# Kernel tuning notes

Measured on AMD Instinct MI355X. Metric: run time of the kernel, lower is better.

## Reference

```python
import jax, jax.numpy as jnp
import numpy as np

K, D, BETA = 512, 64, 0.25


def conv(x, w, b, s, p):
    # x: NCHW, w: OIHW (torch Conv2d layout)
    y = jax.lax.conv_general_dilated(x, w, (s, s), [(p, p), (p, p)],
                                     dimension_numbers=('NCHW', 'OIHW', 'NCHW'))
    if b is not None:
        y = y + b[None, :, None, None]
    return y


def conv_t(x, w, b, s, p):
    # torch ConvTranspose2d: w is (Cin, Cout, k, k). Equivalent to a dilated conv
    # with flipped, transposed kernel and padding k-1-p.
    k = w.shape[2]
    w2 = jnp.transpose(jnp.flip(w, (2, 3)), (1, 0, 2, 3))  # -> (Cout, Cin, k, k)
    y = jax.lax.conv_general_dilated(x, w2, (1, 1), [(k - 1 - p, k - 1 - p)] * 2,
                                     lhs_dilation=(s, s),
                                     dimension_numbers=('NCHW', 'OIHW', 'NCHW'))
    return y + b[None, :, None, None]


def res_stack(x, w1s, w2s):
    # w1s: (n_blocks, C_mid, C_in, 3, 3); w2s: (n_blocks, C_in, C_mid, 1, 1); no bias
    for i in range(w1s.shape[0]):
        h = conv(jax.nn.relu(x), w1s[i], None, 1, 1)
        h = conv(jax.nn.relu(h), w2s[i], None, 1, 0)
        x = x + h
    return jax.nn.relu(x)


def setup_inputs() -> dict:
    key = jax.random.key(0)
    ks = jax.random.split(key, 24)
    rn = lambda k, shape, s=0.05: (jax.random.normal(k, shape, jnp.float32) * s)
    return {
        'x': jax.random.normal(ks[0], (64, 3, 128, 128), jnp.float32),
        'enc_w1': rn(ks[1], (64, 3, 4, 4)),    'enc_b1': rn(ks[2], (64,)),
        'enc_w2': rn(ks[3], (128, 64, 4, 4)),  'enc_b2': rn(ks[4], (128,)),
        'enc_w3': rn(ks[5], (128, 128, 3, 3)), 'enc_b3': rn(ks[6], (128,)),
        'enc_w4': rn(ks[7], (128, 128, 3, 3)), 'enc_b4': rn(ks[8], (128,)),
        'enc_res_w1': rn(ks[9], (2, 64, 128, 3, 3)),
        'enc_res_w2': rn(ks[10], (2, 128, 64, 1, 1)),
        'enc_adj_w': rn(ks[11], (64, 128, 1, 1)), 'enc_adj_b': rn(ks[12], (64,)),
        'E': jax.random.uniform(ks[13], (K, D), jnp.float32, -1.0 / K, 1.0 / K),
        'dec_adj_w': rn(ks[14], (128, 64, 3, 3)), 'dec_adj_b': rn(ks[15], (128,)),
        'dec_res_w1': rn(ks[16], (2, 64, 128, 3, 3)),
        'dec_res_w2': rn(ks[17], (2, 128, 64, 1, 1)),
        'tc1_w': rn(ks[18], (128, 64, 4, 4)), 'tc1_b': rn(ks[19], (64,)),
        'tc2_w': rn(ks[20], (64, 3, 4, 4)),  'tc2_b': rn(ks[21], (3,)),
    }


def vq_vae_forward(x, enc_w1, enc_b1, enc_w2, enc_b2, enc_w3, enc_b3, enc_w4, enc_b4,
                   enc_res_w1, enc_res_w2, enc_adj_w, enc_adj_b, E,
                   dec_adj_w, dec_adj_b, dec_res_w1, dec_res_w2, tc1_w, tc1_b, tc2_w, tc2_b):
    relu = jax.nn.relu
    # ---- Encoder ----
    h = relu(conv(x, enc_w1, enc_b1, 2, 1))      # (B,64,64,64)
    h = relu(conv(h, enc_w2, enc_b2, 2, 1))      # (B,128,32,32)
    h = relu(conv(h, enc_w3, enc_b3, 1, 1))
    h = conv(h, enc_w4, enc_b4, 1, 1)
    h = res_stack(h, enc_res_w1, enc_res_w2)
    Ze = conv(h, enc_adj_w, enc_adj_b, 1, 0)     # (B,D,32,32)
    # ---- Vector quantizer (eval mode, use_EMA=False) ----
    Zt = jnp.transpose(Ze, (0, 2, 3, 1))          # (B,H,W,D)
    flat = Zt.reshape(-1, D)                      # (N,D), N=65536
    dist = (jnp.sum(flat ** 2, axis=1, keepdims=True)
            + jnp.sum(E ** 2, axis=1)
            - 2.0 * flat @ E.T)                    # (N,K)
    idx = jnp.argmin(dist, axis=1)                # (N,)
    Zq = E[idx].reshape(Zt.shape)
    e_latent_loss = jnp.mean((jax.lax.stop_gradient(Zq) - Zt) ** 2)
    q_latent_loss = jnp.mean((Zq - jax.lax.stop_gradient(Zt)) ** 2)
    e_and_q = q_latent_loss + BETA * e_latent_loss
    Zq_st = Zt + jax.lax.stop_gradient(Zq - Zt)   # straight-through
    Zq_nchw = jnp.transpose(Zq_st, (0, 3, 1, 2))
    counts = jnp.zeros((K,), jnp.float32).at[idx].add(1.0)
    probs = counts / jnp.sum(counts)
    entropy_bits = -jnp.sum(probs * jnp.log2(probs + 1e-10))  # zero-count terms vanish
    est_words = 2.0 ** entropy_bits
    # ---- Decoder ----
    g = conv(Zq_nchw, dec_adj_w, dec_adj_b, 1, 1)  # (B,128,32,32)
    g = res_stack(g, dec_res_w1, dec_res_w2)
    g = relu(conv_t(g, tc1_w, tc1_b, 2, 1))        # (B,64,64,64)
    x_recon = conv_t(g, tc2_w, tc2_b, 2, 1)        # (B,3,128,128)
    return e_and_q, x_recon, e_latent_loss, q_latent_loss, est_words


def reference(x, enc_w1, enc_b1, enc_w2, enc_b2, enc_w3, enc_b3, enc_w4, enc_b4,
              enc_res_w1, enc_res_w2, enc_adj_w, enc_adj_b, E,
              dec_adj_w, dec_adj_b, dec_res_w1, dec_res_w2, tc1_w, tc1_b, tc2_w, tc2_b):
    return vq_vae_forward(x, enc_w1, enc_b1, enc_w2, enc_b2, enc_w3, enc_b3, enc_w4, enc_b4,
                          enc_res_w1, enc_res_w2, enc_adj_w, enc_adj_b, E,
                          dec_adj_w, dec_adj_b, dec_res_w1, dec_res_w2, tc1_w, tc1_b, tc2_w, tc2_b)
```

## Files before the change

### kernel.cpp

```cpp
#include <hip/hip_runtime.h>
#include <math.h>


typedef unsigned short u16;
typedef __attribute__((ext_vector_type(8))) short bf16x8;
typedef __attribute__((ext_vector_type(4))) float f32x4;

__device__ __forceinline__ float bf2f(u16 h) {
    union { unsigned u; float f; } v; v.u = ((unsigned)h) << 16; return v.f;
}
__device__ __forceinline__ u16 f2bf(float f) {
    union { float f; unsigned u; } v; v.f = f;
    unsigned r = v.u + 0x7FFFu + ((v.u >> 16) & 1u);
    return (u16)(r >> 16);
}
__device__ __forceinline__ unsigned relu2(unsigned x) {
    return x & ~(((x & 0x80008000u) >> 15) * 0xFFFFu);
}
__device__ __forceinline__ int swz512(int x) {
    return ((x & 7) << 6) | (x >> 3);
}

template<int CIN, int COUT, int TAPMODE, bool RELU_IN, bool RELU_OUT,
         bool HAS_BIAS, bool RESID>
__global__ __launch_bounds__(256)
void mfma_conv_k(const u16* __restrict__ in, const u16* __restrict__ wT,
                 const float* __restrict__ bias, u16* __restrict__ out,
                 int Hin, int Win, int Hout, int Wout, int OS)
{
    constexpr int TM = 2, TN = 4;
    constexpr int LDA = 40;
    constexpr int NCH = CIN / 32;
    constexpr int NTAPS = (TAPMODE == 0) ? 1 : (TAPMODE == 1) ? 9
                        : (TAPMODE == 2) ? 16 : 4;
    constexpr int S = (TAPMODE == 2) ? 2 : 1;

    __shared__ alignas(16) u16 aT[128 * LDA];
    __shared__ alignas(16) u16 bT[64 * LDA];

    const int tid = threadIdx.x;
    const int m0 = swz512(blockIdx.x) * 128;
    const int colbase = blockIdx.y << 6;
    const int pz = (TAPMODE == 3) ? blockIdx.z : 0;
    const u16* wTb = (TAPMODE == 3) ? wT + (size_t)pz * 4 * COUT * CIN : wT;
    const int oph = (TAPMODE == 3) ? (pz >> 1) : 0;
    const int opw = (TAPMODE == 3) ? (pz & 1) : 0;
    const int n_img = m0 >> 10;
    const int pixbase = m0 & 1023;

    const int r = tid >> 1, half = tid & 1;
    const int pr = pixbase + r;
    const int ohr = pr >> 5, owr = pr & 31;
    const u16* inb = in + (size_t)n_img * Hin * Win * CIN;

    const int wv = tid >> 6, lane = tid & 63;
    const int q = lane >> 4, l16 = lane & 15;
    const int mbase = wv * 32;
    const bool bload = r < 64;

    f32x4 acc[TM][TN] = {};

    const int total_it = NTAPS * NCH;
    uint4 pa0, pa1, pb0 = {0,0,0,0}, pb1 = {0,0,0,0};

#define LOAD_IT(IT) do {                                                        \
        int t_ = (IT) / NCH, cc_ = ((IT) % NCH) * 32;                           \
        int dh_, dw_;                                                           \
        if (TAPMODE == 0)      { dh_ = 0;              dw_ = 0; }               \
        else if (TAPMODE == 1) { dh_ = t_/3 - 1;       dw_ = t_%3 - 1; }        \
        else if (TAPMODE == 2) { dh_ = (t_>>2) - 1;    dw_ = (t_&3) - 1; }      \
        else                   { dh_ = (pz>>1) - (t_>>1); dw_ = (pz&1) - (t_&1); } \
        int ih_ = ohr * S + dh_;                                                \
        int iw_ = owr * S + dw_;                                                \
        bool ok_ = ((unsigned)ih_ < (unsigned)Hin) &&                           \
                   ((unsigned)iw_ < (unsigned)Win);                             \
        pa0 = (uint4){0,0,0,0}; pa1 = (uint4){0,0,0,0};                         \
        if (ok_) {                                                              \
            const u16* as_ = inb + ((size_t)ih_ * Win + iw_) * CIN              \
                             + half * 16 + cc_;                                 \
            pa0 = *(const uint4*)(as_);                                         \
            pa1 = *(const uint4*)(as_ + 8);                                     \
        }                                                                       \
        if (bload) {                                                            \
            const u16* bs_ = wTb + ((size_t)t_ * COUT + colbase + r) * CIN      \
                             + half * 16 + cc_;                                 \
            pb0 = *(const uint4*)(bs_);                                         \
            pb1 = *(const uint4*)(bs_ + 8);                                     \
        }                                                                       \
    } while (0)

    LOAD_IT(0);

    for (int it = 0; it < total_it; ++it) {
        __syncthreads();
        uint4 a0 = pa0, a1 = pa1;
        if (RELU_IN) {
            a0.x = relu2(a0.x); a0.y = relu2(a0.y); a0.z = relu2(a0.z); a0.w = relu2(a0.w);
            a1.x = relu2(a1.x); a1.y = relu2(a1.y); a1.z = relu2(a1.z); a1.w = relu2(a1.w);
        }
        *(uint4*)&aT[r * LDA + half * 16]     = a0;
        *(uint4*)&aT[r * LDA + half * 16 + 8] = a1;
        if (bload) {
            *(uint4*)&bT[r * LDA + half * 16]     = pb0;
            *(uint4*)&bT[r * LDA + half * 16 + 8] = pb1;
        }
        __syncthreads();
        if (it + 1 < total_it) LOAD_IT(it + 1);

        bf16x8 afr[TM], bfr[TN];
        #pragma unroll
        for (int tm = 0; tm < TM; ++tm)
            afr[tm] = *(const bf16x8*)&aT[(mbase + tm*16 + l16) * LDA + q * 8];
        #pragma unroll
        for (int tn = 0; tn < TN; ++tn)
            bfr[tn] = *(const bf16x8*)&bT[(tn*16 + l16) * LDA + q * 8];
        #pragma unroll
        for (int tm = 0; tm < TM; ++tm)
            #pragma unroll
            for (int tn = 0; tn < TN; ++tn)
                acc[tm][tn] = __builtin_amdgcn_mfma_f32_16x16x32_bf16(
                    afr[tm], bfr[tn], acc[tm][tn], 0, 0, 0);
    }
#undef LOAD_IT

    #pragma unroll
    for (int tm = 0; tm < TM; ++tm) {
        #pragma unroll
        for (int tn = 0; tn < TN; ++tn) {
            const int col = colbase + tn*16 + l16;
            const float bv = HAS_BIAS ? bias[col] : 0.0f;
            #pragma unroll
            for (int rg = 0; rg < 4; ++rg) {
                const int m = mbase + tm*16 + q*4 + rg;
                const int pix = pixbase + m;
                const int oh = pix >> 5, ow = pix & 31;
                size_t oidx = (((size_t)n_img * Hout + (oh*OS + oph)) * Wout
                               + (ow*OS + opw)) * COUT + col;
                float v = acc[tm][tn][rg] + bv;
                if (RESID) v += bf2f(out[oidx]);
                if (RELU_OUT) v = fmaxf(v, 0.0f);
                out[oidx] = f2bf(v);
            }
        }
    }
}

template<bool FRELU>
__global__ __launch_bounds__(256)
void res_fused_k(const u16* __restrict__ in, const u16* __restrict__ w1,
                 const u16* __restrict__ w2, u16* __restrict__ out)
{
    constexpr int LDA = 40;
    __shared__ alignas(16) u16 smem[20480];
    u16* aT   = smem;
    u16* bT   = smem + 5120;
    u16* mT0  = smem;
    u16* mT1  = smem + 5120;
    u16* b2T0 = smem + 10240;
    u16* b2T1 = smem + 15360;

    const int tid = threadIdx.x;
    const int m0 = swz512(blockIdx.x) * 128;
    const int n_img = m0 >> 10;
    const int pixbase = m0 & 1023;

    const int r = tid >> 1, half = tid & 1;
    const int pr = pixbase + r;
    const int ohr = pr >> 5, owr = pr & 31;
    const u16* inb = in + (size_t)n_img * 1024 * 128;

    const int wv = tid >> 6, lane = tid & 63;
    const int q = lane >> 4, l16 = lane & 15;
    const int mbase = wv * 32;
    const bool bload = r < 64;

    {
        const u16* s = w2 + r * 64 + half * 32;
        u16* d = (half ? b2T1 : b2T0) + r * LDA;
        *(uint4*)(d)      = *(const uint4*)(s);
        *(uint4*)(d + 8)  = *(const uint4*)(s + 8);
        *(uint4*)(d + 16) = *(const uint4*)(s + 16);
        *(uint4*)(d + 24) = *(const uint4*)(s + 24);
    }

    f32x4 acc[2][4] = {};
    uint4 pa0, pa1, pb0 = {0,0,0,0}, pb1 = {0,0,0,0};

#define RLOAD(IT) do {                                                          \
        int t_ = (IT) >> 2, cc_ = ((IT) & 3) * 32;                              \
        int ih_ = ohr + t_/3 - 1, iw_ = owr + t_%3 - 1;                         \
        bool ok_ = ((unsigned)ih_ < 32u) && ((unsigned)iw_ < 32u);              \
        pa0 = (uint4){0,0,0,0}; pa1 = (uint4){0,0,0,0};                         \
        if (ok_) {                                                              \
            const u16* as_ = inb + ((size_t)ih_ * 32 + iw_) * 128               \
                             + half * 16 + cc_;                                 \
            pa0 = *(const uint4*)(as_);                                         \
            pa1 = *(const uint4*)(as_ + 8);                                     \
        }                                                                       \
        if (bload) {                                                            \
            const u16* bs_ = w1 + ((size_t)t_ * 64 + r) * 128                   \
                             + half * 16 + cc_;                                 \
            pb0 = *(const uint4*)(bs_);                                         \
            pb1 = *(const uint4*)(bs_ + 8);                                     \
        }                                                                       \
    } while (0)

    RLOAD(0);
    for (int it = 0; it < 36; ++it) {
        __syncthreads();
        uint4 a0 = pa0, a1 = pa1;
        a0.x = relu2(a0.x); a0.y = relu2(a0.y); a0.z = relu2(a0.z); a0.w = relu2(a0.w);
        a1.x = relu2(a1.x); a1.y = relu2(a1.y); a1.z = relu2(a1.z); a1.w = relu2(a1.w);
        *(uint4*)&aT[r * LDA + half * 16]     = a0;
        *(uint4*)&aT[r * LDA + half * 16 + 8] = a1;
        if (bload) {
            *(uint4*)&bT[r * LDA + half * 16]     = pb0;
            *(uint4*)&bT[r * LDA + half * 16 + 8] = pb1;
        }
        __syncthreads();
        if (it + 1 < 36) RLOAD(it + 1);

        bf16x8 afr[2], bfr[4];
        #pragma unroll
        for (int tm = 0; tm < 2; ++tm)
            afr[tm] = *(const bf16x8*)&aT[(mbase + tm*16 + l16) * LDA + q * 8];
        #pragma unroll
        for (int tn = 0; tn < 4; ++tn)
            bfr[tn] = *(const bf16x8*)&bT[(tn*16 + l16) * LDA + q * 8];
        #pragma unroll
        for (int tm = 0; tm < 2; ++tm)
            #pragma unroll
            for (int tn = 0; tn < 4; ++tn)
                acc[tm][tn] = __builtin_amdgcn_mfma_f32_16x16x32_bf16(
                    afr[tm], bfr[tn], acc[tm][tn], 0, 0, 0);
    }
#undef RLOAD

    __syncthreads();

    #pragma unroll
    for (int tm = 0; tm < 2; ++tm)
        #pragma unroll
        for (int tn = 0; tn < 4; ++tn) {
            u16* dst = (tn < 2) ? mT0 : mT1;
            const int kc = (tn & 1) * 16 + l16;
            #pragma unroll
            for (int rg = 0; rg < 4; ++rg) {
                int row = mbase + tm*16 + q*4 + rg;
                dst[row * LDA + kc] = f2bf(fmaxf(acc[tm][tn][rg], 0.0f));
            }
        }
    __syncthreads();

    f32x4 acc2[2][8] = {};
    #pragma unroll
    for (int kk = 0; kk < 2; ++kk) {
        const u16* mp = kk ? mT1 : mT0;
        const u16* bp = kk ? b2T1 : b2T0;
        bf16x8 af[2], bf[8];
        #pragma unroll
        for (int tm = 0; tm < 2; ++tm)
            af[tm] = *(const bf16x8*)&mp[(mbase + tm*16 + l16) * LDA + q * 8];
        #pragma unroll
        for (int tn = 0; tn < 8; ++tn)
            bf[tn] = *(const bf16x8*)&bp[(tn*16 + l16) * LDA + q * 8];
        #pragma unroll
        for (int tm = 0; tm < 2; ++tm)
            #pragma unroll
            for (int tn = 0; tn < 8; ++tn)
                acc2[tm][tn] = __builtin_amdgcn_mfma_f32_16x16x32_bf16(
                    af[tm], bf[tn], acc2[tm][tn], 0, 0, 0);
    }

    #pragma unroll
    for (int tm = 0; tm < 2; ++tm)
        #pragma unroll
        for (int tn = 0; tn < 8; ++tn) {
            const int col = tn*16 + l16;
            #pragma unroll
            for (int rg = 0; rg < 4; ++rg) {
                const int m = mbase + tm*16 + q*4 + rg;
                const int pix = pixbase + m;
                size_t off = ((size_t)n_img * 1024 + pix) * 128 + col;
                float v = acc2[tm][tn][rg] + bf2f(in[off]);
                if (FRELU) v = fmaxf(v, 0.0f);
                out[off] = f2bf(v);
            }
        }
}

__global__ __launch_bounds__(256)
void adjvq_k(const u16* __restrict__ TRin, const u16* __restrict__ wadj,
             const float* __restrict__ bias, const u16* __restrict__ Ebf,
             const float* __restrict__ enorm1, u16* __restrict__ Zq,
             u16* __restrict__ idx_out, float* __restrict__ sse)
{
    constexpr int LDA = 40;
    __shared__ alignas(16) u16 smem[18432];
    u16* aT  = smem;
    u16* bT  = smem + 5120;
    u16* mT0 = smem;
    u16* mT1 = smem + 5120;
    u16* eld = smem;
    __shared__ float znorm_s[128];
    __shared__ float bestf_s[128];
    __shared__ float en1s[256];
    __shared__ int   bestk_s[128];
    __shared__ float red[256];

    const int tid = threadIdx.x;
    const int r = tid >> 1, half = tid & 1;
    const int bx = swz512(blockIdx.x);
    const size_t gp = (size_t)bx * 128 + r;
    const u16* arow = TRin + gp * 128 + half * 16;
    const u16* brow = wadj + (size_t)r * 128 + half * 16;

    const int wv = tid >> 6, lane = tid & 63;
    const int q = lane >> 4, l16 = lane & 15;
// ... 213 lines not shown
    #pragma unroll
    for (int tm = 0; tm < 2; ++tm) {
        af0[tm] = *(const bf16x8*)&aT0[(mbase + tm*16 + l16) * 40 + q * 8];
        af1[tm] = *(const bf16x8*)&aT1[(mbase + tm*16 + l16) * 40 + q * 8];
    }
    #pragma unroll
    for (int tn = 0; tn < 4; ++tn) {
        bf0[tn] = *(const bf16x8*)&bT0[(tn*16 + l16) * 40 + q * 8];
        bf1[tn] = *(const bf16x8*)&bT1[(tn*16 + l16) * 40 + q * 8];
    }
    #pragma unroll
    for (int tm = 0; tm < 2; ++tm)
        #pragma unroll
        for (int tn = 0; tn < 4; ++tn) {
            acc[tm][tn] = __builtin_amdgcn_mfma_f32_16x16x32_bf16(
                af0[tm], bf0[tn], acc[tm][tn], 0, 0, 0);
            acc[tm][tn] = __builtin_amdgcn_mfma_f32_16x16x32_bf16(
                af1[tm], bf1[tn], acc[tm][tn], 0, 0, 0);
        }

    float bv[4];
    #pragma unroll
    for (int tn = 0; tn < 4; ++tn) bv[tn] = b[tn*16 + l16];

    __syncthreads();
    u16* cbuf = smem;
    #pragma unroll
    for (int tm = 0; tm < 2; ++tm)
        #pragma unroll
        for (int tn = 0; tn < 4; ++tn)
            #pragma unroll
            for (int rg = 0; rg < 4; ++rg) {
                int row = mbase + tm*16 + q*4 + rg;
                int col = tn*16 + l16;
                cbuf[row*72 + col] = f2bf(fmaxf(acc[tm][tn][rg] + bv[tn], 0.0f));
            }
    __syncthreads();

    u16* ob = out + (size_t)gbase * 64;
    #pragma unroll
    for (int it = 0; it < 4; ++it) {
        int j = it * 256 + tid;
        uint4 v = *(const uint4*)&cbuf[(j >> 3) * 72 + (j & 7) * 8];
        *(uint4*)(ob + j * 8) = v;
    }
}

__global__ __launch_bounds__(256)
void tc2_mfma_k(const u16* __restrict__ in, const u16* __restrict__ wT,
                const float* __restrict__ bias, float* __restrict__ out)
{
    constexpr int LDA = 40;
    __shared__ alignas(16) u16 aT[128 * LDA];
    __shared__ alignas(16) u16 bT[16 * LDA];
    __shared__ float cT[128 * 17];

    const int tid = threadIdx.x;
    const int m0 = blockIdx.x * 128;
    const int n_img = m0 >> 12;
    const int pixbase = m0 & 4095;
    const int y0 = pixbase >> 6;

    const int r = tid >> 1, half = tid & 1;
    const int pr = pixbase + r;
    const int yr = pr >> 6, xr = pr & 63;
    const u16* inb = in + (size_t)n_img * 4096 * 64;

    const int wv = tid >> 6, lane = tid & 63;
    const int q = lane >> 4, l16 = lane & 15;
    const int mbase = wv * 32;

    f32x4 acc[2] = {};

    for (int t = 0; t < 9; ++t) {
        const int ih = yr + t/3 - 1;
        const int iw = xr + t%3 - 1;
        const bool ok = ((unsigned)ih < 64u) && ((unsigned)iw < 64u);
        const u16* asrc = ok ? (inb + ((size_t)ih * 64 + iw) * 64 + half * 16) : inb;
        const u16* bsrc = wT + ((size_t)t * 16 + r) * 64 + half * 16;

        for (int c0 = 0; c0 < 64; c0 += 32) {
            __syncthreads();
            uint4 a0 = {0,0,0,0}, a1 = {0,0,0,0};
            if (ok) {
                a0 = *(const uint4*)(asrc + c0);
                a1 = *(const uint4*)(asrc + c0 + 8);
            }
            *(uint4*)&aT[r * LDA + half * 16]     = a0;
            *(uint4*)&aT[r * LDA + half * 16 + 8] = a1;
            if (r < 16) {
                *(uint4*)&bT[r * LDA + half * 16]     = *(const uint4*)(bsrc + c0);
                *(uint4*)&bT[r * LDA + half * 16 + 8] = *(const uint4*)(bsrc + c0 + 8);
            }
            __syncthreads();

            bf16x8 af0 = *(const bf16x8*)&aT[(mbase + l16) * LDA + q * 8];
            bf16x8 af1 = *(const bf16x8*)&aT[(mbase + 16 + l16) * LDA + q * 8];
            bf16x8 bf  = *(const bf16x8*)&bT[l16 * LDA + q * 8];
            acc[0] = __builtin_amdgcn_mfma_f32_16x16x32_bf16(af0, bf, acc[0], 0, 0, 0);
            acc[1] = __builtin_amdgcn_mfma_f32_16x16x32_bf16(af1, bf, acc[1], 0, 0, 0);
        }
    }

    #pragma unroll
    for (int tm = 0; tm < 2; ++tm)
        #pragma unroll
        for (int rg = 0; rg < 4; ++rg)
            cT[(mbase + tm*16 + q*4 + rg) * 17 + l16] = acc[tm][rg];
    __syncthreads();

    #pragma unroll
    for (int it = 0; it < 6; ++it) {
        int j = it * 256 + tid;
        int co  = j >> 9;
        int rem = j & 511;
        int ohl = rem >> 7;
        int ow  = rem & 127;
        int oh  = 2*y0 + ohl;
        int lp  = (ohl >> 1) * 64 + (ow >> 1);
        int col = ((ohl & 1) * 2 + (ow & 1)) * 4 + co;
        float v = cT[lp * 17 + col] + bias[co];
        out[(((size_t)n_img * 3 + co) * 128 + oh) * 128 + ow] = v;
    }
}

__global__ __launch_bounds__(256)
void hist_k(const u16* __restrict__ idx, float* __restrict__ counts)
{
    __shared__ int red[256];
    const int k = blockIdx.x;
    const int tid = threadIdx.x;
    int c = 0;
    const uint4* p4 = (const uint4*)idx;
    for (int i = tid; i < 8192; i += 256) {
        uint4 v = p4[i];
        unsigned ua[4] = {v.x, v.y, v.z, v.w};
        #pragma unroll
        for (int j = 0; j < 4; ++j) {
            c += ((ua[j] & 0xFFFFu) == (unsigned)k);
            c += ((ua[j] >> 16)     == (unsigned)k);
        }
    }
    red[tid] = c;
    __syncthreads();
    for (int s = 128; s > 0; s >>= 1) {
        if (tid < s) red[tid] += red[tid + s];
        __syncthreads();
    }
    if (tid == 0) counts[k] = (float)red[0];
}

__device__ __forceinline__ void wconv_tf(const float* __restrict__ w,
                                         u16* __restrict__ o,
                                         int COUT, int CIN, int KK, int i)
{
    int ci = i % CIN; int t = i / CIN; int co = t % COUT; t /= COUT;
// ... 122 lines not shown
    const float* enc_b2    = (const float*)d_in[4];
    const float* enc_w3    = (const float*)d_in[5];
    const float* enc_b3    = (const float*)d_in[6];
    const float* enc_w4    = (const float*)d_in[7];
    const float* enc_b4    = (const float*)d_in[8];
    const float* enc_res_w1= (const float*)d_in[9];
    const float* enc_res_w2= (const float*)d_in[10];
    const float* enc_adj_w = (const float*)d_in[11];
    const float* enc_adj_b = (const float*)d_in[12];
    const float* Ecb       = (const float*)d_in[13];
    const float* dec_adj_w = (const float*)d_in[14];
    const float* dec_adj_b = (const float*)d_in[15];
    const float* dec_res_w1= (const float*)d_in[16];
    const float* dec_res_w2= (const float*)d_in[17];
    const float* tc1_w     = (const float*)d_in[18];
    const float* tc1_b     = (const float*)d_in[19];
    const float* tc2_w     = (const float*)d_in[20];
    const float* tc2_b     = (const float*)d_in[21];

    char* wsb = (char*)d_ws;
    u16*   wc2   = (u16*)(wsb + 0);
    u16*   wc3   = (u16*)(wsb + 262144);
    u16*   wc4   = (u16*)(wsb + 557056);
    u16*   wer1  = (u16*)(wsb + 851968);
    u16*   wer2  = (u16*)(wsb + 1146880);
    u16*   weadj = (u16*)(wsb + 1179648);
    u16*   wdadj = (u16*)(wsb + 1196032);
    u16*   wdr1  = (u16*)(wsb + 1343488);
    u16*   wdr2  = (u16*)(wsb + 1638400);
    u16*   wtc1  = (u16*)(wsb + 1671168);
    u16*   wtc2b = (u16*)(wsb + 1933312);
    float* counts= (float*)(wsb + 1951744);
    float* sse   = counts + 512;
    u16*   Ebf   = (u16*)(wsb + 1955840);
    float* enorm1= (float*)(wsb + 2021376);
    u16*   wc1b  = (u16*)(wsb + 2023424);
    u16*   H1    = (u16*)(wsb + 2097152);
    u16*   TR    = (u16*)(wsb + 35651584);
    u16*   H3    = (u16*)(wsb + 52428800);
    u16*   ZQ    = (u16*)(wsb + 85983232);
    u16*   IDX   = (u16*)(wsb + 94371840);
    u16*   TC1O  = H1;

    float* out  = (float*)d_out;
    float* xrec = out + 1;
    float* tail = out + 1 + 3145728;

    prep_k<<<3831, 256, 0, stream>>>(enc_w1, enc_w2, enc_w3, enc_w4,
        enc_res_w1, enc_res_w2, dec_res_w1, dec_res_w2, enc_adj_w, dec_adj_w,
        tc1_w, tc2_w, Ecb, wc1b, wc2, wc3, wc4, wer1, wer2, wdr1, wdr2,
        weadj, wdadj, wtc1, wtc2b, Ebf, enorm1, sse);

    conv1_mfma_k<<<2048, 256, 0, stream>>>(x, wc1b, enc_b1, H1);
    mfma_conv_k<64,128,2,false,true,true,false><<<dim3(512,2), 256, 0, stream>>>
        (H1, wc2, enc_b2, TR, 64, 64, 32, 32, 1);
    mfma_conv_k<128,128,1,false,true,true,false><<<dim3(512,2), 256, 0, stream>>>
        (TR, wc3, enc_b3, H3, 32, 32, 32, 32, 1);
    mfma_conv_k<128,128,1,false,false,true,false><<<dim3(512,2), 256, 0, stream>>>
        (H3, wc4, enc_b4, TR, 32, 32, 32, 32, 1);
    res_fused_k<false><<<512, 256, 0, stream>>>(TR, wer1,         wer2,        H3);
    res_fused_k<true ><<<512, 256, 0, stream>>>(H3, wer1 + 73728, wer2 + 8192, TR);

    adjvq_k<<<512, 256, 0, stream>>>(TR, weadj, enc_adj_b, Ebf, enorm1,
                                     ZQ, IDX, sse);
    hist_k<<<512, 256, 0, stream>>>(IDX, counts);

    mfma_conv_k<64,128,1,false,false,true,false><<<dim3(512,2), 256, 0, stream>>>
        (ZQ, wdadj, dec_adj_b, H3, 32, 32, 32, 32, 1);
    res_fused_k<false><<<512, 256, 0, stream>>>(H3, wdr1,         wdr2,        TR);
    res_fused_k<true ><<<512, 256, 0, stream>>>(TR, wdr1 + 73728, wdr2 + 8192, H3);
    mfma_conv_k<128,64,3,false,true,true,false><<<dim3(512,1,4), 256, 0, stream>>>
        (H3, wtc1, tc1_b, TC1O, 32, 32, 64, 64, 2);
    tc2_mfma_k<<<2048, 256, 0, stream>>>(TC1O, wtc2b, tc2_b, xrec);

    finalize_k<<<1, 512, 0, stream>>>(counts, sse, out, tail);
}
```

Baseline: 442.2 us.

## Stage input halo tile in LDS once per channel chunk for 3x3 convs

Replaces the per-tap im2col staging in the 3x3 stride-1 convolutions (encoder conv3/conv4, decoder adjust conv, and the residual blocks' first conv) with a halo tile of 6x34 pixels per 32-channel chunk loaded into LDS once. All 9 taps then read shifted windows from that tile, and weights are read straight from global memory into registers. This cuts redundant global loads of input pixels (about 9x reuse) and the number of barriers per block. In exchange it drops the register prefetch double-buffering, so global loads are no longer overlapped with MFMA work. Weight fragments are fetched from global/L2 in the inner loop.

```diff
diff --git a/kernel.cpp b/kernel.cpp
--- a/kernel.cpp
+++ b/kernel.cpp
@@ -19,6 +19,93 @@
 }
 __device__ __forceinline__ int swz512(int x) {
     return ((x & 7) << 6) | (x >> 3);
+}
+
+template<int CIN, bool RELU_OUT>
+__global__ __launch_bounds__(256)
+void halo3_conv_k(const u16* __restrict__ in, const u16* __restrict__ wT,
+                  const float* __restrict__ bias, u16* __restrict__ out)
+{
+    constexpr int COUT = 128;
+    __shared__ alignas(16) u16 halo[8160];
+
+    const int tid = threadIdx.x;
+    const int m0 = swz512(blockIdx.x) * 128;
+    const int colbase = blockIdx.y << 6;
+    const int n_img = m0 >> 10;
+    const int pixbase = m0 & 1023;
+    const int oh0 = pixbase >> 5;
+    const u16* inb = in + (size_t)n_img * 1024 * CIN;
+
+    const int wv = tid >> 6, lane = tid & 63;
+    const int q = lane >> 4, l16 = lane & 15;
+    const int mbase = wv * 32;
+
+    int abase[2];
+    #pragma unroll
+    for (int tm = 0; tm < 2; ++tm) {
+        int am = mbase + tm*16 + l16;
+        abase[tm] = (((am >> 5) + 1) * 34 + (am & 31) + 1) * 40 + q * 8;
+    }
+
+    f32x4 acc[2][4] = {};
+
+    for (int cc = 0; cc < CIN; cc += 32) {
+        __syncthreads();
+        #pragma unroll
+        for (int j0 = 0; j0 < 1024; j0 += 256) {
+            int j = j0 + tid;
+            if (j < 816) {
+                int cell = j >> 2, part = j & 3;
+                int hr = cell / 34, hc = cell - hr * 34;
+                int ih = oh0 + hr - 1, iw = hc - 1;
+                uint4 v = {0,0,0,0};
+                if (((unsigned)ih < 32u) && ((unsigned)iw < 32u))
+                    v = *(const uint4*)(inb + ((size_t)(ih*32 + iw))*CIN
+                                        + cc + part*8);
+                *(uint4*)&halo[cell*40 + part*8] = v;
+            }
+        }
+        __syncthreads();
+
+        #pragma unroll
+        for (int t = 0; t < 9; ++t) {
+            const int delta = ((t/3 - 1)*34 + (t%3 - 1))*40;
+            bf16x8 bfr[4];
+            #pragma unroll
+            for (int tn = 0; tn < 4; ++tn)
+                bfr[tn] = *(const bf16x8*)(wT
+                    + ((size_t)t*COUT + colbase + tn*16 + l16)*CIN + cc + q*8);
+            bf16x8 afr0 = *(const bf16x8*)&halo[abase[0] + delta];
+            bf16x8 afr1 = *(const bf16x8*)&halo[abase[1] + delta];
+            #pragma unroll
+            for (int tn = 0; tn < 4; ++tn) {
+                acc[0][tn] = __builtin_amdgcn_mfma_f32_16x16x32_bf16(
+                    afr0, bfr[tn], acc[0][tn], 0, 0, 0);
+                acc[1][tn] = __builtin_amdgcn_mfma_f32_16x16x32_bf16(
+                    afr1, bfr[tn], acc[1][tn], 0, 0, 0);
+            }
+        }
+    }
+
+    #pragma unroll
+    for (int tm = 0; tm < 2; ++tm) {
+        #pragma unroll
+        for (int tn = 0; tn < 4; ++tn) {
+            const int col = colbase + tn*16 + l16;
+            const float bv = bias[col];
+            #pragma unroll
+            for (int rg = 0; rg < 4; ++rg) {
+                const int m = mbase + tm*16 + q*4 + rg;
+                const int pix = pixbase + m;
+                const int oh = pix >> 5, ow = pix & 31;
+                size_t oidx = (((size_t)n_img * 32 + oh) * 32 + ow) * COUT + col;
+                float v = acc[tm][tn][rg] + bv;
+                if (RELU_OUT) v = fmaxf(v, 0.0f);
+                out[oidx] = f2bf(v);
+            }
+        }
+    }
 }
 
 template<int CIN, int COUT, int TAPMODE, bool RELU_IN, bool RELU_OUT,
@@ -150,10 +237,8 @@
 void res_fused_k(const u16* __restrict__ in, const u16* __restrict__ w1,
                  const u16* __restrict__ w2, u16* __restrict__ out)
 {
-    constexpr int LDA = 40;
     __shared__ alignas(16) u16 smem[20480];
-    u16* aT   = smem;
-    u16* bT   = smem + 5120;
+    u16* halo = smem;
     u16* mT0  = smem;
     u16* mT1  = smem + 5120;
     u16* b2T0 = smem + 10240;
@@ -163,78 +248,71 @@
     const int m0 = swz512(blockIdx.x) * 128;
     const int n_img = m0 >> 10;
     const int pixbase = m0 & 1023;
-
-    const int r = tid >> 1, half = tid & 1;
-    const int pr = pixbase + r;
-    const int ohr = pr >> 5, owr = pr & 31;
+    const int oh0 = pixbase >> 5;
     const u16* inb = in + (size_t)n_img * 1024 * 128;
 
     const int wv = tid >> 6, lane = tid & 63;
     const int q = lane >> 4, l16 = lane & 15;
     const int mbase = wv * 32;
-    const bool bload = r < 64;
 
     {
+        const int r = tid >> 1, half = tid & 1;
         const u16* s = w2 + r * 64 + half * 32;
-        u16* d = (half ? b2T1 : b2T0) + r * LDA;
+        u16* d = (half ? b2T1 : b2T0) + r * 40;
         *(uint4*)(d)      = *(const uint4*)(s);
         *(uint4*)(d + 8)  = *(const uint4*)(s + 8);
         *(uint4*)(d + 16) = *(const uint4*)(s + 16);
         *(uint4*)(d + 24) = *(const uint4*)(s + 24);
     }
 
+    int abase[2];
+    #pragma unroll
+    for (int tm = 0; tm < 2; ++tm) {
+        int am = mbase + tm*16 + l16;
+        abase[tm] = (((am >> 5) + 1) * 34 + (am & 31) + 1) * 40 + q * 8;
+    }
+
     f32x4 acc[2][4] = {};
-    uint4 pa0, pa1, pb0 = {0,0,0,0}, pb1 = {0,0,0,0};
-
-#define RLOAD(IT) do {                                                          \
-        int t_ = (IT) >> 2, cc_ = ((IT) & 3) * 32;                              \
-        int ih_ = ohr + t_/3 - 1, iw_ = owr + t_%3 - 1;                         \
-        bool ok_ = ((unsigned)ih_ < 32u) && ((unsigned)iw_ < 32u);              \
-        pa0 = (uint4){0,0,0,0}; pa1 = (uint4){0,0,0,0};                         \
-        if (ok_) {                                                              \
-            const u16* as_ = inb + ((size_t)ih_ * 32 + iw_) * 128               \
-                             + half * 16 + cc_;                                 \
-            pa0 = *(const uint4*)(as_);                                         \
-            pa1 = *(const uint4*)(as_ + 8);                                     \
-        }                                                                       \
-        if (bload) {                                                            \
-            const u16* bs_ = w1 + ((size_t)t_ * 64 + r) * 128                   \
-                             + half * 16 + cc_;                                 \
-            pb0 = *(const uint4*)(bs_);                                         \
-            pb1 = *(const uint4*)(bs_ + 8);                                     \
-        }                                                                       \
-    } while (0)
-
-    RLOAD(0);
-    for (int it = 0; it < 36; ++it) {
-        __syncthreads();
-        uint4 a0 = pa0, a1 = pa1;
-        a0.x = relu2(a0.x); a0.y = relu2(a0.y); a0.z = relu2(a0.z); a0.w = relu2(a0.w);
-        a1.x = relu2(a1.x); a1.y = relu2(a1.y); a1.z = relu2(a1.z); a1.w = relu2(a1.w);
-        *(uint4*)&aT[r * LDA + half * 16]     = a0;
-        *(uint4*)&aT[r * LDA + half * 16 + 8] = a1;
-        if (bload) {
-            *(uint4*)&bT[r * LDA + half * 16]     = pb0;
-            *(uint4*)&bT[r * LDA + half * 16 + 8] = pb1;
-        }
-        __syncthreads();
-        if (it + 1 < 36) RLOAD(it + 1);
-
-        bf16x8 afr[2], bfr[4];
-        #pragma unroll
-        for (int tm = 0; tm < 2; ++tm)
-            afr[tm] = *(const bf16x8*)&aT[(mbase + tm*16 + l16) * LDA + q * 8];
-        #pragma unroll
-        for (int tn = 0; tn < 4; ++tn)
-            bfr[tn] = *(const bf16x8*)&bT[(tn*16 + l16) * LDA + q * 8];
-        #pragma unroll
-        for (int tm = 0; tm < 2; ++tm)
+
+    for (int cc = 0; cc < 128; cc += 32) {
+        __syncthreads();
+        #pragma unroll
+        for (int j0 = 0; j0 < 1024; j0 += 256) {
+            int j = j0 + tid;
+            if (j < 816) {
+                int cell = j >> 2, part = j & 3;
+                int hr = cell / 34, hc = cell - hr * 34;
+                int ih = oh0 + hr - 1, iw = hc - 1;
+                uint4 v = {0,0,0,0};
+                if (((unsigned)ih < 32u) && ((unsigned)iw < 32u))
+                    v = *(const uint4*)(inb + ((size_t)(ih*32 + iw))*128
+                                        + cc + part*8);
+                v.x = relu2(v.x); v.y = relu2(v.y);
+                v.z = relu2(v.z); v.w = relu2(v.w);
+                *(uint4*)&halo[cell*40 + part*8] = v;
+            }
+        }
+        __syncthreads();
+
+        #pragma unroll
+        for (int t = 0; t < 9; ++t) {
+            const int delta = ((t/3 - 1)*34 + (t%3 - 1))*40;
+            bf16x8 bfr[4];
             #pragma unroll
             for (int tn = 0; tn < 4; ++tn)
-                acc[tm][tn] = __builtin_amdgcn_mfma_f32_16x16x32_bf16(
-                    afr[tm], bfr[tn], acc[tm][tn], 0, 0, 0);
-    }
-#undef RLOAD
+                bfr[tn] = *(const bf16x8*)(w1
+                    + ((size_t)t*64 + tn*16 + l16)*128 + cc + q*8);
+            bf16x8 afr0 = *(const bf16x8*)&halo[abase[0] + delta];
+            bf16x8 afr1 = *(const bf16x8*)&halo[abase[1] + delta];
+            #pragma unroll
+            for (int tn = 0; tn < 4; ++tn) {
+                acc[0][tn] = __builtin_amdgcn_mfma_f32_16x16x32_bf16(
+                    afr0, bfr[tn], acc[0][tn], 0, 0, 0);
+                acc[1][tn] = __builtin_amdgcn_mfma_f32_16x16x32_bf16(
+                    afr1, bfr[tn], acc[1][tn], 0, 0, 0);
+            }
+        }
+    }
 
     __syncthreads();
 
@@ -247,7 +325,7 @@
             #pragma unroll
             for (int rg = 0; rg < 4; ++rg) {
                 int row = mbase + tm*16 + q*4 + rg;
-                dst[row * LDA + kc] = f2bf(fmaxf(acc[tm][tn][rg], 0.0f));
+                dst[row * 40 + kc] = f2bf(fmaxf(acc[tm][tn][rg], 0.0f));
             }
         }
     __syncthreads();
@@ -260,10 +338,10 @@
         bf16x8 af[2], bf[8];
         #pragma unroll
         for (int tm = 0; tm < 2; ++tm)
-            af[tm] = *(const bf16x8*)&mp[(mbase + tm*16 + l16) * LDA + q * 8];
+            af[tm] = *(const bf16x8*)&mp[(mbase + tm*16 + l16) * 40 + q * 8];
         #pragma unroll
         for (int tn = 0; tn < 8; ++tn)
-            bf[tn] = *(const bf16x8*)&bp[(tn*16 + l16) * LDA + q * 8];
+            bf[tn] = *(const bf16x8*)&bp[(tn*16 + l16) * 40 + q * 8];
         #pragma unroll
         for (int tm = 0; tm < 2; ++tm)
             #pragma unroll
@@ -863,10 +941,8 @@
     conv1_mfma_k<<<2048, 256, 0, stream>>>(x, wc1b, enc_b1, H1);
     mfma_conv_k<64,128,2,false,true,true,false><<<dim3(512,2), 256, 0, stream>>>
         (H1, wc2, enc_b2, TR, 64, 64, 32, 32, 1);
-    mfma_conv_k<128,128,1,false,true,true,false><<<dim3(512,2), 256, 0, stream>>>
-        (TR, wc3, enc_b3, H3, 32, 32, 32, 32, 1);
-    mfma_conv_k<128,128,1,false,false,true,false><<<dim3(512,2), 256, 0, stream>>>
-        (H3, wc4, enc_b4, TR, 32, 32, 32, 32, 1);
+    halo3_conv_k<128,true ><<<dim3(512,2), 256, 0, stream>>>(TR, wc3, enc_b3, H3);
+    halo3_conv_k<128,false><<<dim3(512,2), 256, 0, stream>>>(H3, wc4, enc_b4, TR);
     res_fused_k<false><<<512, 256, 0, stream>>>(TR, wer1,         wer2,        H3);
     res_fused_k<true ><<<512, 256, 0, stream>>>(H3, wer1 + 73728, wer2 + 8192, TR);
 
@@ -874,8 +950,7 @@
                                      ZQ, IDX, sse);
     hist_k<<<512, 256, 0, stream>>>(IDX, counts);
 
-    mfma_conv_k<64,128,1,false,false,true,false><<<dim3(512,2), 256, 0, stream>>>
-        (ZQ, wdadj, dec_adj_b, H3, 32, 32, 32, 32, 1);
+    halo3_conv_k<64,false><<<dim3(512,2), 256, 0, stream>>>(ZQ, wdadj, dec_adj_b, H3);
     res_fused_k<false><<<512, 256, 0, stream>>>(H3, wdr1,         wdr2,        TR);
     res_fused_k<true ><<<512, 256, 0, stream>>>(TR, wdr1 + 73728, wdr2 + 8192, H3);
     mfma_conv_k<128,64,3,false,true,true,false><<<dim3(512,1,4), 256, 0, stream>>>
```

Result: slower. 602.1 us (+36.1%).

## Load weight fragments directly from global into registers, bypassing LDS staging

Applied to the files above, without the earlier changes.

In the generic conv, residual, and tc2 kernels, the B (weight) operand is no longer staged through shared memory. Each lane now loads its MFMA fragments straight from global memory into registers, double-buffered across a K-loop unrolled by two. This cuts LDS stores and reads and the shared-memory footprint. In exchange, every wave loads the same weights redundantly from global or L2, uses more registers, and the main loops still sync twice per iteration.

```diff
diff --git a/kernel.cpp b/kernel.cpp
--- a/kernel.cpp
+++ b/kernel.cpp
@@ -28,15 +28,16 @@
                  const float* __restrict__ bias, u16* __restrict__ out,
                  int Hin, int Win, int Hout, int Wout, int OS)
 {
-    constexpr int TM = 2, TN = 4;
+    constexpr int TM = 2;
     constexpr int LDA = 40;
     constexpr int NCH = CIN / 32;
     constexpr int NTAPS = (TAPMODE == 0) ? 1 : (TAPMODE == 1) ? 9
                         : (TAPMODE == 2) ? 16 : 4;
     constexpr int S = (TAPMODE == 2) ? 2 : 1;
+    constexpr int TOTAL_IT = NTAPS * NCH;
+    static_assert((TOTAL_IT & 1) == 0, "x2-unrolled K-loop needs even count");
 
     __shared__ alignas(16) u16 aT[128 * LDA];
-    __shared__ alignas(16) u16 bT[64 * LDA];
 
     const int tid = threadIdx.x;
     const int m0 = swz512(blockIdx.x) * 128;
@@ -56,14 +57,13 @@
     const int wv = tid >> 6, lane = tid & 63;
     const int q = lane >> 4, l16 = lane & 15;
     const int mbase = wv * 32;
-    const bool bload = r < 64;
-
-    f32x4 acc[TM][TN] = {};
-
-    const int total_it = NTAPS * NCH;
-    uint4 pa0, pa1, pb0 = {0,0,0,0}, pb1 = {0,0,0,0};
-
-#define LOAD_IT(IT) do {                                                        \
+
+    f32x4 acc[TM][4] = {};
+
+    uint4 pa0, pa1;
+    bf16x8 BP0, BP1, BP2, BP3, BQ0, BQ1, BQ2, BQ3;
+
+#define LOAD_A(IT) do {                                                         \
         int t_ = (IT) / NCH, cc_ = ((IT) % NCH) * 32;                           \
         int dh_, dw_;                                                           \
         if (TAPMODE == 0)      { dh_ = 0;              dw_ = 0; }               \
@@ -81,52 +81,71 @@
             pa0 = *(const uint4*)(as_);                                         \
             pa1 = *(const uint4*)(as_ + 8);                                     \
         }                                                                       \
-        if (bload) {                                                            \
-            const u16* bs_ = wTb + ((size_t)t_ * COUT + colbase + r) * CIN      \
-                             + half * 16 + cc_;                                 \
-            pb0 = *(const uint4*)(bs_);                                         \
-            pb1 = *(const uint4*)(bs_ + 8);                                     \
+    } while (0)
+
+#define LOADB(IT, B0, B1, B2, B3) do {                                          \
+        int t_ = (IT) / NCH, cc_ = ((IT) % NCH) * 32;                           \
+        const u16* wb_ = wTb + ((size_t)t_ * COUT + colbase + l16) * CIN        \
+                         + cc_ + q * 8;                                         \
+        B0 = *(const bf16x8*)(wb_);                                             \
+        B1 = *(const bf16x8*)(wb_ + (size_t)16 * CIN);                          \
+        B2 = *(const bf16x8*)(wb_ + (size_t)32 * CIN);                          \
+        B3 = *(const bf16x8*)(wb_ + (size_t)48 * CIN);                          \
+    } while (0)
+
+#define STAGE_A() do {                                                          \
+        uint4 a0 = pa0, a1 = pa1;                                               \
+        if (RELU_IN) {                                                          \
+            a0.x = relu2(a0.x); a0.y = relu2(a0.y);                             \
+            a0.z = relu2(a0.z); a0.w = relu2(a0.w);                             \
+            a1.x = relu2(a1.x); a1.y = relu2(a1.y);                             \
+            a1.z = relu2(a1.z); a1.w = relu2(a1.w);                             \
         }                                                                       \
+        *(uint4*)&aT[r * LDA + half * 16]     = a0;                             \
+        *(uint4*)&aT[r * LDA + half * 16 + 8] = a1;                             \
     } while (0)
 
-    LOAD_IT(0);
-
-    for (int it = 0; it < total_it; ++it) {
-        __syncthreads();
-        uint4 a0 = pa0, a1 = pa1;
-        if (RELU_IN) {
-            a0.x = relu2(a0.x); a0.y = relu2(a0.y); a0.z = relu2(a0.z); a0.w = relu2(a0.w);
-            a1.x = relu2(a1.x); a1.y = relu2(a1.y); a1.z = relu2(a1.z); a1.w = relu2(a1.w);
-        }
-        *(uint4*)&aT[r * LDA + half * 16]     = a0;
-        *(uint4*)&aT[r * LDA + half * 16 + 8] = a1;
-        if (bload) {
-            *(uint4*)&bT[r * LDA + half * 16]     = pb0;
-            *(uint4*)&bT[r * LDA + half * 16 + 8] = pb1;
-        }
-        __syncthreads();
-        if (it + 1 < total_it) LOAD_IT(it + 1);
-
-        bf16x8 afr[TM], bfr[TN];
-        #pragma unroll
-        for (int tm = 0; tm < TM; ++tm)
-            afr[tm] = *(const bf16x8*)&aT[(mbase + tm*16 + l16) * LDA + q * 8];
-        #pragma unroll
-        for (int tn = 0; tn < TN; ++tn)
-            bfr[tn] = *(const bf16x8*)&bT[(tn*16 + l16) * LDA + q * 8];
-        #pragma unroll
-        for (int tm = 0; tm < TM; ++tm)
-            #pragma unroll
-            for (int tn = 0; tn < TN; ++tn)
-                acc[tm][tn] = __builtin_amdgcn_mfma_f32_16x16x32_bf16(
-                    afr[tm], bfr[tn], acc[tm][tn], 0, 0, 0);
-    }
-#undef LOAD_IT
+#define DO_MFMA(B0, B1, B2, B3) do {                                            \
+        bf16x8 af0 = *(const bf16x8*)&aT[(mbase + l16) * LDA + q * 8];          \
+        bf16x8 af1 = *(const bf16x8*)&aT[(mbase + 16 + l16) * LDA + q * 8];     \
+        acc[0][0] = __builtin_amdgcn_mfma_f32_16x16x32_bf16(af0, B0, acc[0][0], 0, 0, 0); \
+        acc[0][1] = __builtin_amdgcn_mfma_f32_16x16x32_bf16(af0, B1, acc[0][1], 0, 0, 0); \
+        acc[0][2] = __builtin_amdgcn_mfma_f32_16x16x32_bf16(af0, B2, acc[0][2], 0, 0, 0); \
+        acc[0][3] = __builtin_amdgcn_mfma_f32_16x16x32_bf16(af0, B3, acc[0][3], 0, 0, 0); \
+        acc[1][0] = __builtin_amdgcn_mfma_f32_16x16x32_bf16(af1, B0, acc[1][0], 0, 0, 0); \
+        acc[1][1] = __builtin_amdgcn_mfma_f32_16x16x32_bf16(af1, B1, acc[1][1], 0, 0, 0); \
+        acc[1][2] = __builtin_amdgcn_mfma_f32_16x16x32_bf16(af1, B2, acc[1][2], 0, 0, 0); \
+        acc[1][3] = __builtin_amdgcn_mfma_f32_16x16x32_bf16(af1, B3, acc[1][3], 0, 0, 0); \
+    } while (0)
+
+    LOAD_A(0);
+    LOADB(0, BP0, BP1, BP2, BP3);
+
+    for (int it = 0; it < TOTAL_IT; it += 2) {
+        __syncthreads();
+        STAGE_A();
+        __syncthreads();
+        LOAD_A(it + 1);
+        LOADB(it + 1, BQ0, BQ1, BQ2, BQ3);
+        DO_MFMA(BP0, BP1, BP2, BP3);
+        __syncthreads();
+        STAGE_A();
+        __syncthreads();
+        if (it + 2 < TOTAL_IT) {
+            LOAD_A(it + 2);
+            LOADB(it + 2, BP0, BP1, BP2, BP3);
+        }
+        DO_MFMA(BQ0, BQ1, BQ2, BQ3);
+    }
+#undef DO_MFMA
+#undef STAGE_A
+#undef LOADB
+#undef LOAD_A
 
     #pragma unroll
     for (int tm = 0; tm < TM; ++tm) {
         #pragma unroll
-        for (int tn = 0; tn < TN; ++tn) {
+        for (int tn = 0; tn < 4; ++tn) {
             const int col = colbase + tn*16 + l16;
             const float bv = HAS_BIAS ? bias[col] : 0.0f;
             #pragma unroll
@@ -153,7 +172,6 @@
     constexpr int LDA = 40;
     __shared__ alignas(16) u16 smem[20480];
     u16* aT   = smem;
-    u16* bT   = smem + 5120;
     u16* mT0  = smem;
     u16* mT1  = smem + 5120;
     u16* b2T0 = smem + 10240;
@@ -172,7 +190,6 @@
     const int wv = tid >> 6, lane = tid & 63;
     const int q = lane >> 4, l16 = lane & 15;
     const int mbase = wv * 32;
-    const bool bload = r < 64;
 
     {
         const u16* s = w2 + r * 64 + half * 32;
@@ -184,9 +201,10 @@
     }
 
     f32x4 acc[2][4] = {};
-    uint4 pa0, pa1, pb0 = {0,0,0,0}, pb1 = {0,0,0,0};
-
-#define RLOAD(IT) do {                                                          \
+    uint4 pa0, pa1;
+    bf16x8 BP0, BP1, BP2, BP3, BQ0, BQ1, BQ2, BQ3;
+
+#define RLOAD_A(IT) do {                                                        \
         int t_ = (IT) >> 2, cc_ = ((IT) & 3) * 32;                              \
         int ih_ = ohr + t_/3 - 1, iw_ = owr + t_%3 - 1;                         \
         bool ok_ = ((unsigned)ih_ < 32u) && ((unsigned)iw_ < 32u);              \
@@ -197,44 +215,64 @@
             pa0 = *(const uint4*)(as_);                                         \
             pa1 = *(const uint4*)(as_ + 8);                                     \
         }                                                                       \
-        if (bload) {                                                            \
-            const u16* bs_ = w1 + ((size_t)t_ * 64 + r) * 128                   \
-                             + half * 16 + cc_;                                 \
-            pb0 = *(const uint4*)(bs_);                                         \
-            pb1 = *(const uint4*)(bs_ + 8);                                     \
-        }                                                                       \
     } while (0)
 
-    RLOAD(0);
-    for (int it = 0; it < 36; ++it) {
-        __syncthreads();
-        uint4 a0 = pa0, a1 = pa1;
-        a0.x = relu2(a0.x); a0.y = relu2(a0.y); a0.z = relu2(a0.z); a0.w = relu2(a0.w);
-        a1.x = relu2(a1.x); a1.y = relu2(a1.y); a1.z = relu2(a1.z); a1.w = relu2(a1.w);
-        *(uint4*)&aT[r * LDA + half * 16]     = a0;
-        *(uint4*)&aT[r * LDA + half * 16 + 8] = a1;
-        if (bload) {
-            *(uint4*)&bT[r * LDA + half * 16]     = pb0;
-            *(uint4*)&bT[r * LDA + half * 16 + 8] = pb1;
-        }
-        __syncthreads();
-        if (it + 1 < 36) RLOAD(it + 1);
-
-        bf16x8 afr[2], bfr[4];
-        #pragma unroll
-        for (int tm = 0; tm < 2; ++tm)
-            afr[tm] = *(const bf16x8*)&aT[(mbase + tm*16 + l16) * LDA + q * 8];
-        #pragma unroll
-        for (int tn = 0; tn < 4; ++tn)
-            bfr[tn] = *(const bf16x8*)&bT[(tn*16 + l16) * LDA + q * 8];
-        #pragma unroll
-        for (int tm = 0; tm < 2; ++tm)
-            #pragma unroll
-            for (int tn = 0; tn < 4; ++tn)
-                acc[tm][tn] = __builtin_amdgcn_mfma_f32_16x16x32_bf16(
-                    afr[tm], bfr[tn], acc[tm][tn], 0, 0, 0);
-    }
-#undef RLOAD
+#define RLOADB(IT, B0, B1, B2, B3) do {                                         \
+        int t_ = (IT) >> 2, cc_ = ((IT) & 3) * 32;                              \
+        const u16* wb_ = w1 + ((size_t)t_ * 64 + l16) * 128 + cc_ + q * 8;      \
+        B0 = *(const bf16x8*)(wb_);                                             \
+        B1 = *(const bf16x8*)(wb_ + (size_t)16 * 128);                          \
+        B2 = *(const bf16x8*)(wb_ + (size_t)32 * 128);                          \
+        B3 = *(const bf16x8*)(wb_ + (size_t)48 * 128);                          \
+    } while (0)
+
+#define RSTAGE_A() do {                                                         \
+        uint4 a0 = pa0, a1 = pa1;                                               \
+        a0.x = relu2(a0.x); a0.y = relu2(a0.y);                                 \
+        a0.z = relu2(a0.z); a0.w = relu2(a0.w);                                 \
+        a1.x = relu2(a1.x); a1.y = relu2(a1.y);                                 \
+        a1.z = relu2(a1.z); a1.w = relu2(a1.w);                                 \
+        *(uint4*)&aT[r * LDA + half * 16]     = a0;                             \
+        *(uint4*)&aT[r * LDA + half * 16 + 8] = a1;                             \
+    } while (0)
+
+#define RDO_MFMA(B0, B1, B2, B3) do {                                           \
+        bf16x8 af0 = *(const bf16x8*)&aT[(mbase + l16) * LDA + q * 8];          \
+        bf16x8 af1 = *(const bf16x8*)&aT[(mbase + 16 + l16) * LDA + q * 8];     \
+        acc[0][0] = __builtin_amdgcn_mfma_f32_16x16x32_bf16(af0, B0, acc[0][0], 0, 0, 0); \
+        acc[0][1] = __builtin_amdgcn_mfma_f32_16x16x32_bf16(af0, B1, acc[0][1], 0, 0, 0); \
+        acc[0][2] = __builtin_amdgcn_mfma_f32_16x16x32_bf16(af0, B2, acc[0][2], 0, 0, 0); \
+        acc[0][3] = __builtin_amdgcn_mfma_f32_16x16x32_bf16(af0, B3, acc[0][3], 0, 0, 0); \
+        acc[1][0] = __builtin_amdgcn_mfma_f32_16x16x32_bf16(af1, B0, acc[1][0], 0, 0, 0); \
+        acc[1][1] = __builtin_amdgcn_mfma_f32_16x16x32_bf16(af1, B1, acc[1][1], 0, 0, 0); \
+        acc[1][2] = __builtin_amdgcn_mfma_f32_16x16x32_bf16(af1, B2, acc[1][2], 0, 0, 0); \
+        acc[1][3] = __builtin_amdgcn_mfma_f32_16x16x32_bf16(af1, B3, acc[1][3], 0, 0, 0); \
+    } while (0)
+
+    RLOAD_A(0);
+    RLOADB(0, BP0, BP1, BP2, BP3);
+
+    for (int it = 0; it < 36; it += 2) {
+        __syncthreads();
+        RSTAGE_A();
+        __syncthreads();
+        RLOAD_A(it + 1);
+        RLOADB(it + 1, BQ0, BQ1, BQ2, BQ3);
+        RDO_MFMA(BP0, BP1, BP2, BP3);
+
+        __syncthreads();
+        RSTAGE_A();
+        __syncthreads();
+        if (it + 2 < 36) {
+            RLOAD_A(it + 2);
+            RLOADB(it + 2, BP0, BP1, BP2, BP3);
+        }
+        RDO_MFMA(BQ0, BQ1, BQ2, BQ3);
+    }
+#undef RDO_MFMA
+#undef RSTAGE_A
+#undef RLOADB
+#undef RLOAD_A
 
     __syncthreads();
 
@@ -583,7 +621,6 @@
 {
     constexpr int LDA = 40;
     __shared__ alignas(16) u16 aT[128 * LDA];
-    __shared__ alignas(16) u16 bT[16 * LDA];
     __shared__ float cT[128 * 17];
 
     const int tid = threadIdx.x;
@@ -608,9 +645,10 @@
         const int iw = xr + t%3 - 1;
         const bool ok = ((unsigned)ih < 64u) && ((unsigned)iw < 64u);
         const u16* asrc = ok ? (inb + ((size_t)ih * 64 + iw) * 64 + half * 16) : inb;
-        const u16* bsrc = wT + ((size_t)t * 16 + r) * 64 + half * 16;
 
         for (int c0 = 0; c0 < 64; c0 += 32) {
+            bf16x8 bf = *(const bf16x8*)(wT + ((size_t)t * 16 + l16) * 64
+                                         + c0 + q * 8);
             __syncthreads();
             uint4 a0 = {0,0,0,0}, a1 = {0,0,0,0};
             if (ok) {
@@ -619,20 +657,16 @@
             }
             *(uint4*)&aT[r * LDA + half * 16]     = a0;
             *(uint4*)&aT[r * LDA + half * 16 + 8] = a1;
-            if (r < 16) {
-                *(uint4*)&bT[r * LDA + half * 16]     = *(const uint4*)(bsrc + c0);
-                *(uint4*)&bT[r * LDA + half * 16 + 8] = *(const uint4*)(bsrc + c0 + 8);
-            }
             __syncthreads();
 
             bf16x8 af0 = *(const bf16x8*)&aT[(mbase + l16) * LDA + q * 8];
             bf16x8 af1 = *(const bf16x8*)&aT[(mbase + 16 + l16) * LDA + q * 8];
-            bf16x8 bf  = *(const bf16x8*)&bT[l16 * LDA + q * 8];
             acc[0] = __builtin_amdgcn_mfma_f32_16x16x32_bf16(af0, bf, acc[0], 0, 0, 0);
             acc[1] = __builtin_amdgcn_mfma_f32_16x16x32_bf16(af1, bf, acc[1], 0, 0, 0);
         }
     }
 
+    __syncthreads();
     #pragma unroll
     for (int tm = 0; tm < 2; ++tm)
         #pragma unroll
```

Measured after the change: 741.6 us. 1.68x slower.

## Add 512-thread conv kernel computing all 128 output channels per block

Applied to the files above, without the earlier changes.

Adds a new MFMA conv kernel that uses 512 threads and a 128x128 output tile, so each block covers all output channels instead of splitting them across two blocks in grid y. Each input pixel tile is now loaded once rather than twice, which cuts redundant global loads of activations. It also uses register prefetch of the next iteration's loads to overlap memory with compute. The trade-off is half as many blocks, larger shared memory per block, and possibly lower occupancy.

```diff
diff --git a/kernel.cpp b/kernel.cpp
--- a/kernel.cpp
+++ b/kernel.cpp
@@ -19,6 +19,105 @@
 }
 __device__ __forceinline__ int swz512(int x) {
     return ((x & 7) << 6) | (x >> 3);
+}
+
+template<int CIN, int TAPMODE, bool RELU_OUT>
+__global__ __launch_bounds__(512)
+void mfma_conv512_k(const u16* __restrict__ in, const u16* __restrict__ wT,
+                    const float* __restrict__ bias, u16* __restrict__ out,
+                    int Hin, int Win, int Hout, int Wout)
+{
+    constexpr int COUT = 128;
+    constexpr int LDA = 40;
+    constexpr int NCH = CIN / 32;
+    constexpr int NTAPS = (TAPMODE == 0) ? 1 : (TAPMODE == 1) ? 9 : 16;
+    constexpr int S = (TAPMODE == 2) ? 2 : 1;
+
+    __shared__ alignas(16) u16 aT[128 * LDA];
+    __shared__ alignas(16) u16 bT[128 * LDA];
+
+    const int tid = threadIdx.x;
+    const int m0 = swz512(blockIdx.x) * 128;
+    const int n_img = m0 >> 10;
+    const int pixbase = m0 & 1023;
+
+    const int r = tid >> 2, part = tid & 3;
+    const int pr = pixbase + r;
+    const int ohr = pr >> 5, owr = pr & 31;
+    const u16* inb = in + (size_t)n_img * Hin * Win * CIN;
+
+    const int wv = tid >> 6, lane = tid & 63;
+    const int q = lane >> 4, l16 = lane & 15;
+    const int mbase = (wv & 3) * 32;
+    const int colbase = (wv >> 2) * 64;
+
+    f32x4 acc[2][4] = {};
+
+    const int total_it = NTAPS * NCH;
+    uint4 pa, pb;
+
+#define LOAD_IT(IT) do {                                                        \
+        int t_ = (IT) / NCH, cc_ = ((IT) % NCH) * 32;                           \
+        int dh_, dw_;                                                           \
+        if (TAPMODE == 0)      { dh_ = 0;           dw_ = 0; }                  \
+        else if (TAPMODE == 1) { dh_ = t_/3 - 1;    dw_ = t_%3 - 1; }           \
+        else                   { dh_ = (t_>>2) - 1; dw_ = (t_&3) - 1; }         \
+        int ih_ = ohr * S + dh_;                                                \
+        int iw_ = owr * S + dw_;                                                \
+        bool ok_ = ((unsigned)ih_ < (unsigned)Hin) &&                           \
+                   ((unsigned)iw_ < (unsigned)Win);                             \
+        pa = (uint4){0,0,0,0};                                                  \
+        if (ok_)                                                                \
+            pa = *(const uint4*)(inb + ((size_t)ih_ * Win + iw_) * CIN          \
+                                 + cc_ + part * 8);                             \
+        pb = *(const uint4*)(wT + ((size_t)t_ * COUT + r) * CIN                 \
+                             + cc_ + part * 8);                                 \
+    } while (0)
+
+    LOAD_IT(0);
+
+    for (int it = 0; it < total_it; ++it) {
+        __syncthreads();
+        *(uint4*)&aT[r * LDA + part * 8] = pa;
+        *(uint4*)&bT[r * LDA + part * 8] = pb;
+        __syncthreads();
+        if (it + 1 < total_it) LOAD_IT(it + 1);
+
+        bf16x8 afr[2], bfr[4];
+        #pragma unroll
+        for (int tm = 0; tm < 2; ++tm)
+            afr[tm] = *(const bf16x8*)&aT[(mbase + tm*16 + l16) * LDA + q * 8];
+        #pragma unroll
+        for (int tn = 0; tn < 4; ++tn)
+            bfr[tn] = *(const bf16x8*)&bT[(colbase + tn*16 + l16) * LDA + q * 8];
+        #pragma unroll
+        for (int tm = 0; tm < 2; ++tm)
+            #pragma unroll
+            for (int tn = 0; tn < 4; ++tn)
+                acc[tm][tn] = __builtin_amdgcn_mfma_f32_16x16x32_bf16(
+                    afr[tm], bfr[tn], acc[tm][tn], 0, 0, 0);
+    }
+#undef LOAD_IT
+
+    #pragma unroll
+    for (int tm = 0; tm < 2; ++tm) {
+        #pragma unroll
+        for (int tn = 0; tn < 4; ++tn) {
+            const int col = colbase + tn*16 + l16;
+            const float bv = bias[col];
+            #pragma unroll
+            for (int rg = 0; rg < 4; ++rg) {
+                const int m = mbase + tm*16 + q*4 + rg;
+                const int pix = pixbase + m;
+                const int oh = pix >> 5, ow = pix & 31;
+                size_t oidx = (((size_t)n_img * Hout + oh) * Wout + ow) * COUT
+                              + col;
+                float v = acc[tm][tn][rg] + bv;
+                if (RELU_OUT) v = fmaxf(v, 0.0f);
+                out[oidx] = f2bf(v);
+            }
+        }
+    }
 }
 
 template<int CIN, int COUT, int TAPMODE, bool RELU_IN, bool RELU_OUT,
@@ -861,12 +960,12 @@
         weadj, wdadj, wtc1, wtc2b, Ebf, enorm1, sse);
 
     conv1_mfma_k<<<2048, 256, 0, stream>>>(x, wc1b, enc_b1, H1);
-    mfma_conv_k<64,128,2,false,true,true,false><<<dim3(512,2), 256, 0, stream>>>
-        (H1, wc2, enc_b2, TR, 64, 64, 32, 32, 1);
-    mfma_conv_k<128,128,1,false,true,true,false><<<dim3(512,2), 256, 0, stream>>>
-        (TR, wc3, enc_b3, H3, 32, 32, 32, 32, 1);
-    mfma_conv_k<128,128,1,false,false,true,false><<<dim3(512,2), 256, 0, stream>>>
-        (H3, wc4, enc_b4, TR, 32, 32, 32, 32, 1);
+    mfma_conv512_k<64,2,true ><<<512, 512, 0, stream>>>
+        (H1, wc2, enc_b2, TR, 64, 64, 32, 32);
+    mfma_conv512_k<128,1,true ><<<512, 512, 0, stream>>>
+        (TR, wc3, enc_b3, H3, 32, 32, 32, 32);
+    mfma_conv512_k<128,1,false><<<512, 512, 0, stream>>>
+        (H3, wc4, enc_b4, TR, 32, 32, 32, 32);
     res_fused_k<false><<<512, 256, 0, stream>>>(TR, wer1,         wer2,        H3);
     res_fused_k<true ><<<512, 256, 0, stream>>>(H3, wer1 + 73728, wer2 + 8192, TR);
 
@@ -874,8 +973,8 @@
                                      ZQ, IDX, sse);
     hist_k<<<512, 256, 0, stream>>>(IDX, counts);
 
-    mfma_conv_k<64,128,1,false,false,true,false><<<dim3(512,2), 256, 0, stream>>>
-        (ZQ, wdadj, dec_adj_b, H3, 32, 32, 32, 32, 1);
+    mfma_conv512_k<64,1,false><<<512, 512, 0, stream>>>
+        (ZQ, wdadj, dec_adj_b, H3, 32, 32, 32, 32);
     res_fused_k<false><<<512, 256, 0, stream>>>(H3, wdr1,         wdr2,        TR);
     res_fused_k<true ><<<512, 256, 0, stream>>>(TR, wdr1 + 73728, wdr2 + 8192, H3);
     mfma_conv_k<128,64,3,false,true,true,false><<<dim3(512,1,4), 256, 0, stream>>>
```

Measured after the change: 434.5 us. About the same (-1.8%).
